# Performance work log

Hardware: AMD Instinct MI355X
Metric: run time of the kernel (lower is better)

## Reference

```python
import jax, jax.numpy as jnp
import numpy as np

OUT = 4096       # out_features
IN = 4096        # in_features
GS = 128         # group_size
G = IN // GS     # num_groups = 32 (IN divisible by GS -> no padding path)


def setup_inputs() -> dict:
    key = jax.random.key(0)
    k1, k2, k3 = jax.random.split(key, 3)
    x = jax.random.normal(k1, (4096, IN), dtype=jnp.float32)
    # packed int4 weights: each byte holds two 4-bit codes in [0,15] (offset-8)
    qweight = jax.random.randint(k2, (OUT, IN // 2), 0, 256, dtype=jnp.int32)
    # per-(row, group) positive scales
    scale = jax.random.uniform(k3, (OUT, G, 1), dtype=jnp.float32,
                               minval=0.01, maxval=0.1)
    return {"x": x, "qweight": qweight, "scale": scale}


def reference(x, qweight, scale):
    # unpack_int4: high nibble is the even-position element, low nibble odd
    high = (qweight >> 4) & 15
    low = qweight & 15
    q = jnp.stack([high, low], axis=-1).reshape(OUT, -1)  # [OUT, IN]
    q = q.astype(jnp.float32) - 8.0                       # back to [-8, 7]
    # group-wise dequantization
    w = q.reshape(OUT, G, GS) * scale                     # [OUT, G, GS]
    B = x.shape[0]
    xg = x.reshape(B, G, GS)                              # [B, G, GS]
    return jnp.einsum('bgs,ogs->bo', xg, w)               # [B, OUT]
```

## Files before the change

kernel.cpp:

```cpp
#include <hip/hip_runtime.h>

typedef __attribute__((ext_vector_type(8))) _Float16 f16x8;
typedef __attribute__((ext_vector_type(4))) float    f32x4;
typedef __attribute__((ext_vector_type(4))) int      i32x4;

#define IN_F   4096
#define OUT_F  4096
#define NGRP   32
#define NKT    64

#define GLOAD16(gsrc, ldst)                                                   \
    __builtin_amdgcn_global_load_lds(                                         \
        (const __attribute__((address_space(1))) unsigned int*)(gsrc),        \
        (__attribute__((address_space(3))) unsigned int*)(ldst), 16, 0, 0)

#define CFENCE  asm volatile("" ::: "memory")
#define BARRIER do { CFENCE; __builtin_amdgcn_s_barrier(); CFENCE; } while (0)
#define VMW6    asm volatile("s_waitcnt vmcnt(6)" ::: "memory")

__global__ __launch_bounds__(256)
void prep(const float* __restrict__ X, const int* __restrict__ QW,
          const float* __restrict__ S, _Float16* __restrict__ XF,
          _Float16* __restrict__ WF) {
    if (blockIdx.x < 8192) {
        size_t i = ((size_t)blockIdx.x * 256 + threadIdx.x) * 8;
        f32x4 a = *(const f32x4*)(X + i);
        f32x4 b = *(const f32x4*)(X + i + 4);
        f16x8 h;
        h[0] = (_Float16)a[0]; h[1] = (_Float16)a[1];
        h[2] = (_Float16)a[2]; h[3] = (_Float16)a[3];
        h[4] = (_Float16)b[0]; h[5] = (_Float16)b[1];
        h[6] = (_Float16)b[2]; h[7] = (_Float16)b[3];
        *(f16x8*)(XF + i) = h;
    } else {
        size_t t  = ((size_t)blockIdx.x - 8192) * 256 + threadIdx.x;
        size_t jj = t * 4;
        size_t o  = jj >> 11;
        size_t jr = jj & 2047;
        const float s = S[o * NGRP + (jr >> 6)];
        i32x4 q = *(const i32x4*)(QW + jj);
        f16x8 h;
#pragma unroll
        for (int j = 0; j < 4; ++j) {
            const int v = q[j];
            h[2 * j]     = (_Float16)((float)(((v >> 4) & 15) - 8) * s);
            h[2 * j + 1] = (_Float16)((float)((v & 15) - 8) * s);
        }
        *(f16x8*)(WF + jj * 2) = h;
    }
}

__global__ __launch_bounds__(512, 2)
void gemm8p(const _Float16* __restrict__ A,
            const _Float16* __restrict__ B,
            float*          __restrict__ C)
{
    extern __shared__ char LDSc[];
    char* const ldsA = LDSc;
    char* const ldsB = LDSc + 65536;

    const int tid  = threadIdx.x;
    const int lane = tid & 63;
    const int wid  = tid >> 6;
    const int wm   = wid >> 2;
    const int wn   = wid & 3;

    const int bid = blockIdx.x;
    const int swz = (bid & 7) * 32 + (bid >> 3);
    const int bm0 = (swz >> 4) * 256;
    const int bn0 = (swz & 15) * 256;

    const int r0 = tid >> 3;
    const int cs = ((tid & 7) * 16) ^ ((r0 & 7) << 4);
    const _Float16* Asrc = A + (size_t)(bm0 + r0) * IN_F + (cs >> 1);
    const _Float16* Bsrc = B + (size_t)(bn0 + r0) * IN_F + (cs >> 1);
    const int dstoff = wid * 1024;

    const int lane15 = lane & 15;
    const int swr = (lane & 7) << 4;
    const int c0 = ((lane >> 4) * 16) ^ swr;
    const int c1 = (64 + (lane >> 4) * 16) ^ swr;
    int rAoff[4], rBoff[2];
#pragma unroll
    for (int mm = 0; mm < 4; ++mm) rAoff[mm] = (wm * 64 + mm * 16 + lane15) * 128;
#pragma unroll
    for (int nn = 0; nn < 2; ++nn) rBoff[nn] = (wn * 32 + nn * 16 + lane15) * 128;

    f16x8 afr[4][2], blo[2][2], bhi[2][2];
    f32x4 acc[8][4];
#pragma unroll
    for (int m = 0; m < 8; ++m)
#pragma unroll
        for (int n = 0; n < 4; ++n) acc[m][n] = (f32x4)0.0f;

#define STAGE_A(HALF, KT, BUF) do {                                           \
        const _Float16* s_ = Asrc + (size_t)(HALF) * 128 * IN_F + (KT) * 64;  \
        char* d_ = ldsA + ((BUF) * 2 + (HALF)) * 16384 + dstoff;              \
        GLOAD16(s_, d_);                                                      \
        GLOAD16(s_ + (size_t)64 * IN_F, d_ + 8192); } while (0)

#define STAGE_B(HALF, KT, BUF) do {                                           \
        const _Float16* s_ = Bsrc + (size_t)(HALF) * 128 * IN_F + (KT) * 64;  \
        char* d_ = ldsB + ((BUF) * 2 + (HALF)) * 16384 + dstoff;              \
        GLOAD16(s_, d_);                                                      \
        GLOAD16(s_ + (size_t)64 * IN_F, d_ + 8192); } while (0)

#define RD_A(BUF, QM) do { char* ab_ = ldsA + ((BUF) * 2 + (QM)) * 16384;     \
        _Pragma("unroll") for (int mm = 0; mm < 4; ++mm) {                    \
            afr[mm][0] = *(const f16x8*)(ab_ + rAoff[mm] + c0);               \
            afr[mm][1] = *(const f16x8*)(ab_ + rAoff[mm] + c1); } } while (0)

#define RD_B(BUF, QN, DST) do { char* bb_ = ldsB + ((BUF) * 2 + (QN)) * 16384;\
        _Pragma("unroll") for (int nn = 0; nn < 2; ++nn) {                    \
            DST[nn][0] = *(const f16x8*)(bb_ + rBoff[nn] + c0);               \
            DST[nn][1] = *(const f16x8*)(bb_ + rBoff[nn] + c1); } } while (0)

#define MFMA_Q(QM, QN, BQ)                                                    \
        __builtin_amdgcn_s_setprio(1);                                        \
        _Pragma("unroll") for (int mm = 0; mm < 4; ++mm)                      \
        _Pragma("unroll") for (int nn = 0; nn < 2; ++nn)                      \
        _Pragma("unroll") for (int kk = 0; kk < 2; ++kk)                      \
            acc[(QM)*4+mm][(QN)*2+nn] =                                       \
                __builtin_amdgcn_mfma_f32_16x16x32_f16(                       \
                    afr[mm][kk], BQ[nn][kk], acc[(QM)*4+mm][(QN)*2+nn],0,0,0);\
        __builtin_amdgcn_s_setprio(0);

    STAGE_A(0, 0, 0); STAGE_B(0, 0, 0); STAGE_B(1, 0, 0); STAGE_A(1, 0, 0);
    STAGE_A(0, 1, 1); STAGE_B(0, 1, 1); STAGE_B(1, 1, 1);
    VMW6; BARRIER;

    for (int t = 0; t < NKT; t += 2) {
        const int k2 = (t + 2) & 63;
        const int k3 = (t + 3) & 63;
        RD_A(0, 0); RD_B(0, 0, blo); STAGE_A(1, t + 1, 1);
        MFMA_Q(0, 0, blo); BARRIER;
        RD_B(0, 1, bhi); STAGE_A(0, k2, 0);
        MFMA_Q(0, 1, bhi); BARRIER;
        RD_A(0, 1); STAGE_B(0, k2, 0);
        MFMA_Q(1, 0, blo); BARRIER;
        STAGE_B(1, k2, 0);
        MFMA_Q(1, 1, bhi); VMW6; BARRIER;
        RD_A(1, 0); RD_B(1, 0, blo); STAGE_A(1, k2, 0);
        MFMA_Q(0, 0, blo); BARRIER;
        RD_B(1, 1, bhi); STAGE_A(0, k3, 1);
        MFMA_Q(0, 1, bhi); BARRIER;
        RD_A(1, 1); STAGE_B(0, k3, 1);
        MFMA_Q(1, 0, blo); BARRIER;
        STAGE_B(1, k3, 1);
        MFMA_Q(1, 1, bhi); VMW6; BARRIER;
    }
    asm volatile("s_waitcnt vmcnt(0)" ::: "memory");

#pragma unroll
    for (int m = 0; m < 8; ++m) {
        const int Mr = bm0 + (m >> 2) * 128 + wm * 64 + (m & 3) * 16 + (lane >> 4) * 4;
#pragma unroll
        for (int n = 0; n < 4; ++n) {
            const int Nc = bn0 + (n >> 1) * 128 + wn * 32 + (n & 1) * 16 + lane15;
#pragma unroll
            for (int r = 0; r < 4; ++r)
                C[(size_t)(Mr + r) * OUT_F + Nc] = acc[m][n][r];
        }
    }
#undef STAGE_A
#undef STAGE_B
#undef RD_A
#undef RD_B
#undef MFMA_Q
}

__global__ __launch_bounds__(256, 3)
void gemm_f16(const _Float16* __restrict__ A,
              const _Float16* __restrict__ B,
              float*          __restrict__ C)
{
    __shared__ __align__(16) _Float16 lA[128 * 32];
    __shared__ __align__(16) _Float16 lB[128 * 32];

    const int tid  = threadIdx.x;
    const int lane = tid & 63;
    const int bid = blockIdx.x;
    const int swz = (bid & 7) * 128 + (bid >> 3);
    const int bm0 = (swz >> 5) * 128;
    const int bn0 = (swz & 31) * 128;

    const int sr = tid >> 2;
    const int sc = (tid & 3) * 8;
    const _Float16* Aps = A + (size_t)(bm0 + sr) * IN_F + sc;
    const _Float16* Bps = B + (size_t)(bn0 + sr) * IN_F + sc;
    char* lAb = (char*)lA + (tid & ~63) * 16;
    char* lBb = (char*)lB + (tid & ~63) * 16;

    const int wv = tid >> 6;
    const int wr = (wv >> 1) * 64;
    const int wc = (wv & 1)  * 64;
    const int lr  = lane & 15;
    const int lkb = (lane >> 4) * 16;

    f32x4 acc[4][4];
#pragma unroll
    for (int m = 0; m < 4; ++m)
#pragma unroll
        for (int n = 0; n < 4; ++n) acc[m][n] = (f32x4)0.0f;

    for (int kt = 0; kt < 128; ++kt) {
        __syncthreads();
        {
            const _Float16* ak = Aps + kt * 32;
            const _Float16* bk = Bps + kt * 32;
            GLOAD16(ak, lAb);
            GLOAD16(ak + (size_t)64 * IN_F, lAb + 4096);
            GLOAD16(bk, lBb);
            GLOAD16(bk + (size_t)64 * IN_F, lBb + 4096);
        }
        __syncthreads();

        f16x8 a[4], b[4];
#pragma unroll
        for (int m = 0; m < 4; ++m)
            a[m] = *(const f16x8*)((const char*)lA + (wr + m * 16 + lr) * 64 + lkb);
#pragma unroll
        for (int n = 0; n < 4; ++n)
            b[n] = *(const f16x8*)((const char*)lB + (wc + n * 16 + lr) * 64 + lkb);
#pragma unroll
        for (int m = 0; m < 4; ++m)
#pragma unroll
            for (int n = 0; n < 4; ++n)
                acc[m][n] = __builtin_amdgcn_mfma_f32_16x16x32_f16(
                    a[m], b[n], acc[m][n], 0, 0, 0);
    }

    const int crow = bm0 + wr + (lane >> 4) * 4;
    const int ccol = bn0 + wc + lr;
#pragma unroll
    for (int m = 0; m < 4; ++m)
#pragma unroll
        for (int n = 0; n < 4; ++n)
#pragma unroll
            for (int r = 0; r < 4; ++r)
                C[(size_t)(crow + m * 16 + r) * OUT_F + (ccol + n * 16)]
                    = acc[m][n][r];
}

extern "C" void kernel_launch(void* const* d_in, const int* in_sizes, int n_in,
                              void* d_out, int out_size, void* d_ws, size_t ws_size,
                              hipStream_t stream) {
    (void)in_sizes; (void)n_in; (void)out_size; (void)ws_size;
    const float* x  = (const float*)d_in[0];
    const int*   qw = (const int*)d_in[1];
    const float* s  = (const float*)d_in[2];
    float*       out = (float*)d_out;

    _Float16* xf = (_Float16*)d_ws;
    _Float16* wf = xf + (size_t)OUT_F * IN_F;
    prep<<<dim3(16384), dim3(256), 0, stream>>>(x, qw, s, xf, wf);

    hipError_t e = hipFuncSetAttribute((const void*)gemm8p,
        hipFuncAttributeMaxDynamicSharedMemorySize, 131072);
    if (e == hipSuccess)
        gemm8p<<<dim3(256), dim3(512), 131072, stream>>>(xf, wf, out);
    else
        gemm_f16<<<dim3(1024), dim3(256), 0, stream>>>(xf, wf, out);
}
```

Measured before the change: 135.7 us.

## Software-pipeline LDS fragment reads one MFMA quadrant ahead with double A fragments

```diff
diff --git a/kernel.cpp b/kernel.cpp
--- a/kernel.cpp
+++ b/kernel.cpp
@@ -16,7 +16,8 @@
 
 #define CFENCE  asm volatile("" ::: "memory")
 #define BARRIER do { CFENCE; __builtin_amdgcn_s_barrier(); CFENCE; } while (0)
-#define VMW6    asm volatile("s_waitcnt vmcnt(6)" ::: "memory")
+#define VMW4    asm volatile("s_waitcnt vmcnt(4)" ::: "memory")
+#define SCHED0  __builtin_amdgcn_sched_barrier(0)
 
 __global__ __launch_bounds__(256)
 void prep(const float* __restrict__ X, const int* __restrict__ QW,
@@ -86,7 +87,7 @@
 #pragma unroll
     for (int nn = 0; nn < 2; ++nn) rBoff[nn] = (wn * 32 + nn * 16 + lane15) * 128;
 
-    f16x8 afr[4][2], blo[2][2], bhi[2][2];
+    f16x8 afr[4][2], afr2[4][2], blo[2][2], bhi[2][2];
     f32x4 acc[8][4];
 #pragma unroll
     for (int m = 0; m < 8; ++m)
@@ -105,49 +106,50 @@
         GLOAD16(s_, d_);                                                      \
         GLOAD16(s_ + (size_t)64 * IN_F, d_ + 8192); } while (0)
 
-#define RD_A(BUF, QM) do { char* ab_ = ldsA + ((BUF) * 2 + (QM)) * 16384;     \
+#define RD_A(BUF, QM, DST) do { char* ab_ = ldsA + ((BUF) * 2 + (QM)) * 16384;\
         _Pragma("unroll") for (int mm = 0; mm < 4; ++mm) {                    \
-            afr[mm][0] = *(const f16x8*)(ab_ + rAoff[mm] + c0);               \
-            afr[mm][1] = *(const f16x8*)(ab_ + rAoff[mm] + c1); } } while (0)
+            DST[mm][0] = *(const f16x8*)(ab_ + rAoff[mm] + c0);               \
+            DST[mm][1] = *(const f16x8*)(ab_ + rAoff[mm] + c1); } } while (0)
 
 #define RD_B(BUF, QN, DST) do { char* bb_ = ldsB + ((BUF) * 2 + (QN)) * 16384;\
         _Pragma("unroll") for (int nn = 0; nn < 2; ++nn) {                    \
             DST[nn][0] = *(const f16x8*)(bb_ + rBoff[nn] + c0);               \
             DST[nn][1] = *(const f16x8*)(bb_ + rBoff[nn] + c1); } } while (0)
 
-#define MFMA_Q(QM, QN, BQ)                                                    \
+#define MFMA_Q(QM, QN, AQ, BQ)                                                \
         __builtin_amdgcn_s_setprio(1);                                        \
         _Pragma("unroll") for (int mm = 0; mm < 4; ++mm)                      \
         _Pragma("unroll") for (int nn = 0; nn < 2; ++nn)                      \
         _Pragma("unroll") for (int kk = 0; kk < 2; ++kk)                      \
             acc[(QM)*4+mm][(QN)*2+nn] =                                       \
                 __builtin_amdgcn_mfma_f32_16x16x32_f16(                       \
-                    afr[mm][kk], BQ[nn][kk], acc[(QM)*4+mm][(QN)*2+nn],0,0,0);\
+                    AQ[mm][kk], BQ[nn][kk], acc[(QM)*4+mm][(QN)*2+nn],0,0,0); \
         __builtin_amdgcn_s_setprio(0);
 
     STAGE_A(0, 0, 0); STAGE_B(0, 0, 0); STAGE_B(1, 0, 0); STAGE_A(1, 0, 0);
     STAGE_A(0, 1, 1); STAGE_B(0, 1, 1); STAGE_B(1, 1, 1);
-    VMW6; BARRIER;
+    asm volatile("s_waitcnt vmcnt(6)" ::: "memory"); BARRIER;
+    RD_A(0, 0, afr); RD_B(0, 0, blo);
 
     for (int t = 0; t < NKT; t += 2) {
         const int k2 = (t + 2) & 63;
         const int k3 = (t + 3) & 63;
-        RD_A(0, 0); RD_B(0, 0, blo); STAGE_A(1, t + 1, 1);
-        MFMA_Q(0, 0, blo); BARRIER;
-        RD_B(0, 1, bhi); STAGE_A(0, k2, 0);
-        MFMA_Q(0, 1, bhi); BARRIER;
-        RD_A(0, 1); STAGE_B(0, k2, 0);
-        MFMA_Q(1, 0, blo); BARRIER;
-        STAGE_B(1, k2, 0);
-        MFMA_Q(1, 1, bhi); VMW6; BARRIER;
-        RD_A(1, 0); RD_B(1, 0, blo); STAGE_A(1, k2, 0);
-        MFMA_Q(0, 0, blo); BARRIER;
-        RD_B(1, 1, bhi); STAGE_A(0, k3, 1);
-        MFMA_Q(0, 1, bhi); BARRIER;
-        RD_A(1, 1); STAGE_B(0, k3, 1);
-        MFMA_Q(1, 0, blo); BARRIER;
-        STAGE_B(1, k3, 1);
-        MFMA_Q(1, 1, bhi); VMW6; BARRIER;
+        RD_B(0, 1, bhi); STAGE_A(1, t + 1, 1);
+        SCHED0; MFMA_Q(0, 0, afr, blo); BARRIER;
+        RD_A(0, 1, afr2); STAGE_A(0, k2, 0);
+        SCHED0; MFMA_Q(0, 1, afr, bhi); BARRIER;
+        STAGE_B(0, k2, 0);
+        SCHED0; MFMA_Q(1, 0, afr2, blo); VMW4; BARRIER;
+        RD_A(1, 0, afr); RD_B(1, 0, blo); STAGE_B(1, k2, 0);
+        SCHED0; MFMA_Q(1, 1, afr2, bhi); BARRIER;
+        RD_B(1, 1, bhi); STAGE_A(1, k2, 0);
+        SCHED0; MFMA_Q(0, 0, afr, blo); BARRIER;
+        RD_A(1, 1, afr2); STAGE_A(0, k3, 1);
+        SCHED0; MFMA_Q(0, 1, afr, bhi); BARRIER;
+        STAGE_B(0, k3, 1);
+        SCHED0; MFMA_Q(1, 0, afr2, blo); VMW4; BARRIER;
+        RD_A(0, 0, afr); RD_B(0, 0, blo); STAGE_B(1, k3, 1);
+        SCHED0; MFMA_Q(1, 1, afr2, bhi); BARRIER;
     }
     asm volatile("s_waitcnt vmcnt(0)" ::: "memory");
 
```

Result: slower. 147.2 us (+8.5%).

## Halve barriers per k-step by merging MFMA quadrants into two phases

Applied to the files above, without the earlier changes.

```diff
diff --git a/kernel.cpp b/kernel.cpp
--- a/kernel.cpp
+++ b/kernel.cpp
@@ -132,22 +132,22 @@
     for (int t = 0; t < NKT; t += 2) {
         const int k2 = (t + 2) & 63;
         const int k3 = (t + 3) & 63;
-        RD_A(0, 0); RD_B(0, 0, blo); STAGE_A(1, t + 1, 1);
-        MFMA_Q(0, 0, blo); BARRIER;
-        RD_B(0, 1, bhi); STAGE_A(0, k2, 0);
-        MFMA_Q(0, 1, bhi); BARRIER;
-        RD_A(0, 1); STAGE_B(0, k2, 0);
-        MFMA_Q(1, 0, blo); BARRIER;
-        STAGE_B(1, k2, 0);
-        MFMA_Q(1, 1, bhi); VMW6; BARRIER;
-        RD_A(1, 0); RD_B(1, 0, blo); STAGE_A(1, k2, 0);
-        MFMA_Q(0, 0, blo); BARRIER;
-        RD_B(1, 1, bhi); STAGE_A(0, k3, 1);
-        MFMA_Q(0, 1, bhi); BARRIER;
-        RD_A(1, 1); STAGE_B(0, k3, 1);
-        MFMA_Q(1, 0, blo); BARRIER;
-        STAGE_B(1, k3, 1);
-        MFMA_Q(1, 1, bhi); VMW6; BARRIER;
+        RD_A(0, 0); RD_B(0, 0, blo); RD_B(0, 1, bhi);
+        STAGE_A(1, t + 1, 1);
+        MFMA_Q(0, 0, blo); MFMA_Q(0, 1, bhi);
+        BARRIER;
+        RD_A(0, 1);
+        STAGE_A(0, k2, 0); STAGE_B(0, k2, 0); STAGE_B(1, k2, 0);
+        MFMA_Q(1, 0, blo); MFMA_Q(1, 1, bhi);
+        VMW6; BARRIER;
+        RD_A(1, 0); RD_B(1, 0, blo); RD_B(1, 1, bhi);
+        STAGE_A(1, k2, 0);
+        MFMA_Q(0, 0, blo); MFMA_Q(0, 1, bhi);
+        BARRIER;
+        RD_A(1, 1);
+        STAGE_A(0, k3, 1); STAGE_B(0, k3, 1); STAGE_B(1, k3, 1);
+        MFMA_Q(1, 0, blo); MFMA_Q(1, 1, bhi);
+        VMW6; BARRIER;
     }
     asm volatile("s_waitcnt vmcnt(0)" ::: "memory");
 
```

New measurement: 135.4 us, median of 4. Within noise of the previous version (-0.2%).
